# Kernel optimization log

Measured on AMD Instinct MI355X. Metric: run time of the kernel, lower is better.

The kernel has to match this reference:

```python
import jax, jax.numpy as jnp
import numpy as np

W_BITS = 4  # active precision (max of supported_bits)
EPS = 0.005  # clamp margin from the original module


def _dequant_kbit(qweight, lut, w_bits):
    """Bit-plane LUT dequant.
    qweight: [w_bits, O, I//32] int32, plane b holds bit b (MSB-first code) of each
    weight's k-bit index, 32 consecutive input positions per int32 word (LSB-first
    within a word). lut: [O, 2**w_bits]. Returns dense weight [O, I].
    """
    O = qweight.shape[1]
    shifts = jnp.arange(32, dtype=jnp.int32)                     # bit position within word
    bits = (qweight[:, :, :, None] >> shifts) & 1                # [w_bits, O, I//32, 32]
    plane_w = (1 << (w_bits - 1 - jnp.arange(w_bits, dtype=jnp.int32)))
    idx = (bits * plane_w[:, None, None, None]).sum(axis=0)      # [O, I//32, 32]
    idx = idx.reshape(O, -1)                                     # [O, I]
    return jnp.take_along_axis(lut, idx, axis=1)                 # [O, I]


def _csr_dense(rows, cols, vals, O, I):
    """Scatter CSR (indptr=rows) into a dense [O, I] matrix."""
    nnz = cols.shape[0]
    k = jnp.arange(nnz, dtype=rows.dtype)
    row_ids = jnp.searchsorted(rows, k, side='right') - 1        # CSR row of each nnz
    return jnp.zeros((O, I), dtype=vals.dtype).at[row_ids, cols].add(vals)


def setup_inputs() -> dict:
    key = jax.random.key(0)
    ks = jax.random.split(key, 7)
    B, S, I, O = 4, 2048, 4096, 4096
    NNZ = 65536
    x = jax.random.normal(ks[0], (B, S, I), dtype=jnp.float32)
    qweight = jax.random.randint(ks[1], (W_BITS, O, I // 32), 0, 2147483647, dtype=jnp.int32)
    lut = jax.random.normal(ks[2], (O, 2 ** W_BITS), dtype=jnp.float32) * 0.05
    rows = jnp.sort(jax.random.randint(ks[3], (O + 1,), 0, NNZ, dtype=jnp.int32))
    rows = rows.at[0].set(0).at[-1].set(NNZ)                     # valid CSR indptr
    cols = jax.random.randint(ks[4], (NNZ,), 0, I, dtype=jnp.int32)
    vals = jax.random.normal(ks[5], (NNZ,), dtype=jnp.float32) * 0.01
    bias = jax.random.normal(ks[6], (O,), dtype=jnp.float32) * 0.01
    return {"x": x, "qweight": qweight, "lut": lut, "rows": rows,
            "cols": cols, "vals": vals, "bias": bias}


def reference(x, qweight, lut, rows, cols, vals, bias):
    O = qweight.shape[1]
    I = x.shape[-1]
    weight = _dequant_kbit(qweight, lut, W_BITS)                 # [O, I]
    y = jnp.einsum('bsi,oi->bso', x, weight)                     # dense quantized GEMM
    w_sp = _csr_dense(rows, cols, vals, O, I)                    # sparse outlier weights
    y = y + jnp.einsum('bsi,oi->bso', x, w_sp)
    y = y + bias
    fmax = jnp.finfo(x.dtype).max * (1.0 - EPS)
    return jnp.clip(y, -fmax, fmax)
```

## Files before the change

kernel.cpp:

```cpp
#include <hip/hip_runtime.h>
#include <stdint.h>

#define Mdim 8192
#define Ndim 4096
#define Kdim 4096

#define BM 256
#define BN 256
#define BK 64
#define NT2 (Kdim / BK)

typedef float f32x4 __attribute__((ext_vector_type(4)));
typedef __bf16 bf16x8 __attribute__((ext_vector_type(8)));
typedef unsigned short ushort_t;

#define FMAXC 3.3858093490333422e+38f

__device__ __forceinline__ ushort_t f2bf(float f) {
    unsigned u = __float_as_uint(f);
    u += 0x7fffu + ((u >> 16) & 1u);
    return (ushort_t)(u >> 16);
}

__device__ __forceinline__ void gload_lds16(const void* g, void* l) {
    __builtin_amdgcn_global_load_lds(
        (const __attribute__((address_space(1))) uint32_t*)g,
        (__attribute__((address_space(3))) uint32_t*)(uint32_t)(uintptr_t)l,
        16, 0, 0);
}

#define SGB(mask, n) __builtin_amdgcn_sched_group_barrier(mask, n, 0)

__global__ __launch_bounds__(128) void dequant_kernel(
        const int* __restrict__ qw, const float* __restrict__ lut,
        const int* __restrict__ rows, const int* __restrict__ cols,
        const float* __restrict__ vals, ushort_t* __restrict__ w16) {
    __shared__ float wrow[128 * 33];
    __shared__ float slut[16];
    const int o = blockIdx.x;
    const int t = threadIdx.x;

    if (t < 16) slut[t] = lut[o * 16 + t];
    __syncthreads();

    const int q0 = qw[0 * Ndim * 128 + o * 128 + t];
    const int q1 = qw[1 * Ndim * 128 + o * 128 + t];
    const int q2 = qw[2 * Ndim * 128 + o * 128 + t];
    const int q3 = qw[3 * Ndim * 128 + o * 128 + t];
    float* dst = &wrow[t * 33];
#pragma unroll
    for (int j = 0; j < 32; ++j) {
        int idx = (((q0 >> j) & 1) << 3) | (((q1 >> j) & 1) << 2) |
                  (((q2 >> j) & 1) << 1) | ((q3 >> j) & 1);
        dst[j] = slut[idx];
    }
    __syncthreads();

    const int beg = rows[o], end = rows[o + 1];
    for (int k = beg + t; k < end; k += 128) {
        int c = cols[k];
        atomicAdd(&wrow[c + (c >> 5)], vals[k]);
    }
    __syncthreads();

    __align__(16) ushort_t tmp[32];
#pragma unroll
    for (int j = 0; j < 32; ++j) tmp[j] = f2bf(dst[j]);
    uint4* dstg = (uint4*)(w16 + (size_t)o * Kdim + t * 32);
    const uint4* srcg = (const uint4*)tmp;
#pragma unroll
    for (int j = 0; j < 4; ++j) dstg[j] = srcg[j];
}

__global__ __launch_bounds__(256) void convx_kernel(
        const float* __restrict__ x, ushort_t* __restrict__ y) {
    size_t i = ((size_t)blockIdx.x * 256 + threadIdx.x) * 8;
    float4 a = *(const float4*)(x + i);
    float4 b = *(const float4*)(x + i + 4);
    __align__(16) ushort_t r[8] = {f2bf(a.x), f2bf(a.y), f2bf(a.z), f2bf(a.w),
                                   f2bf(b.x), f2bf(b.y), f2bf(b.z), f2bf(b.w)};
    *(uint4*)(y + i) = *(const uint4*)r;
}

__global__ __launch_bounds__(512, 2) void gemm_kernel(
        const ushort_t* __restrict__ A, const ushort_t* __restrict__ Bw,
        const float* __restrict__ bias, float* __restrict__ C) {
    __shared__ __align__(16) char lds[131072];

    const int wgid = blockIdx.x;
    const int swz = (wgid & 7) * 64 + (wgid >> 3);
    const int bn = swz & 15, bm = swz >> 4;
    const int m0 = bm * BM, n0 = bn * BN;

    const int tid = threadIdx.x;
    const int lane = tid & 63, wid = tid >> 6;
    const int wr = wid >> 2, wc = wid & 3;
    const int fr = lane & 15, kg = lane >> 4;

    const int srow = tid >> 3;
    const int scol = (((tid & 7) ^ (srow & 7)) * 8);
    const ushort_t* gA = A + (size_t)(m0 + srow) * Kdim + scol;
    const ushort_t* gB = Bw + (size_t)(n0 + srow) * Kdim + scol;

    const int off0 = fr * 128 + (((kg) ^ (fr & 7)) << 4);
    const int off1 = fr * 128 + (((4 | kg) ^ (fr & 7)) << 4);

    f32x4 acc[8][4];
#pragma unroll
    for (int i = 0; i < 8; ++i)
#pragma unroll
        for (int j = 0; j < 4; ++j) acc[i][j] = (f32x4){0.f, 0.f, 0.f, 0.f};

    auto stage = [&](int buf, int t1) {
        const ushort_t* sa = gA + (size_t)t1 * BK;
        const ushort_t* sb = gB + (size_t)t1 * BK;
        char* da = lds + buf * 65536 + tid * 16;
        char* db = da + 32768;
#pragma unroll
        for (int j = 0; j < 4; ++j) {
            gload_lds16(sa + (size_t)j * 64 * Kdim, da + j * 8192);
            gload_lds16(sb + (size_t)j * 64 * Kdim, db + j * 8192);
        }
    };
    auto readA = [&](bf16x8 (&FA)[8], const char* Ab, int off) {
#pragma unroll
        for (int m = 0; m < 8; ++m)
            FA[m] = *(const bf16x8*)(Ab + wr * 16384 + m * 2048 + off);
    };
    auto readB = [&](bf16x8 (&FB)[4], const char* Bb, int off) {
#pragma unroll
        for (int n = 0; n < 4; ++n)
            FB[n] = *(const bf16x8*)(Bb + wc * 8192 + n * 2048 + off);
    };
    auto mfmaK = [&](bf16x8 (&FA)[8], bf16x8 (&FB)[4]) {
#pragma unroll
        for (int m = 0; m < 8; ++m)
#pragma unroll
            for (int n = 0; n < 4; ++n)
                acc[m][n] = __builtin_amdgcn_mfma_f32_16x16x32_bf16(
                    FA[m], FB[n], acc[m][n], 0, 0, 0);
    };

    stage(0, 0);
    asm volatile("s_waitcnt vmcnt(0)");
    __builtin_amdgcn_sched_barrier(0);
    __builtin_amdgcn_s_barrier();

#pragma unroll 1
    for (int t = 0; t < NT2 - 1; ++t) {
        const char* Ab = lds + (t & 1) * 65536;
        const char* Bb = Ab + 32768;

        bf16x8 A0[8], B0[4], A1[8], B1[4];
        readA(A0, Ab, off0); readB(B0, Bb, off0);
        stage((t + 1) & 1, t + 1);
        readA(A1, Ab, off1); readB(B1, Bb, off1);

        __builtin_amdgcn_s_setprio(1);
        mfmaK(A0, B0);
        mfmaK(A1, B1);
        __builtin_amdgcn_s_setprio(0);

        SGB(0x100, 12);
#pragma unroll
        for (int i = 0; i < 4; ++i) { SGB(0x30, 2); SGB(0x8, 4); }
#pragma unroll
        for (int i = 0; i < 6; ++i) { SGB(0x100, 2); SGB(0x8, 2); }
        SGB(0x8, 36);

        asm volatile("s_waitcnt vmcnt(0)");
        __builtin_amdgcn_sched_barrier(0);
        __builtin_amdgcn_s_barrier();
    }

    {
        const char* Ab = lds + ((NT2 - 1) & 1) * 65536;
        const char* Bb = Ab + 32768;
        bf16x8 A0[8], B0[4], A1[8], B1[4];
        readA(A0, Ab, off0); readB(B0, Bb, off0);
        readA(A1, Ab, off1); readB(B1, Bb, off1);
        mfmaK(A0, B0);
        mfmaK(A1, B1);
    }

    const int rg = lane >> 4;
#pragma unroll
    for (int nf = 0; nf < 4; ++nf) {
        const int col = n0 + wc * 64 + nf * 16 + fr;
        const float bv = bias[col];
#pragma unroll
        for (int mf = 0; mf < 8; ++mf) {
            const int row = m0 + wr * 128 + mf * 16 + rg * 4;
            float* outp = C + (size_t)row * Ndim + col;
#pragma unroll
            for (int j = 0; j < 4; ++j) {
                float v = acc[mf][nf][j] + bv;
                v = fminf(fmaxf(v, -FMAXC), FMAXC);
                outp[(size_t)j * Ndim] = v;
            }
        }
    }
}

extern "C" void kernel_launch(void* const* d_in, const int* in_sizes, int n_in,
                              void* d_out, int out_size, void* d_ws, size_t ws_size,
                              hipStream_t stream) {
    const float* x    = (const float*)d_in[0];
    const int*   qw   = (const int*)d_in[1];
    const float* lut  = (const float*)d_in[2];
    const int*   rows = (const int*)d_in[3];
    const int*   cols = (const int*)d_in[4];
    const float* vals = (const float*)d_in[5];
    const float* bias = (const float*)d_in[6];
    float* out = (float*)d_out;

    ushort_t* x16 = (ushort_t*)d_ws;
    ushort_t* w16 = x16 + (size_t)Mdim * Kdim;

    hipLaunchKernelGGL(dequant_kernel, dim3(Ndim), dim3(128), 0, stream,
                       qw, lut, rows, cols, vals, w16);
    hipLaunchKernelGGL(convx_kernel, dim3((Mdim * Kdim) / (256 * 8)), dim3(256), 0, stream,
                       x, x16);
    hipLaunchKernelGGL(gemm_kernel, dim3((Mdim / BM) * (Ndim / BN)), dim3(512), 0, stream,
                       x16, w16, bias, out);
}
```

Baseline: 275.7 us.

## Pre-swizzle activations into MFMA fragment order and load A directly to registers

The conversion kernel now writes bf16 activations in MFMA fragment-major order, so each lane's 16-byte A fragment is contiguous per 16x32 tile. The GEMM loads A fragments straight from global memory into registers, double-buffered across half-tiles, and keeps only B in LDS. LDS use drops from 128KB to 64KB and the A LDS traffic goes away. In exchange the A reads now depend on global/L2 latency hidden by register prefetch, register pressure rises, and the hand-tuned schedule-group barriers are replaced.

```diff
diff --git a/kernel.cpp b/kernel.cpp
--- a/kernel.cpp
+++ b/kernel.cpp
@@ -74,18 +74,25 @@
 
 __global__ __launch_bounds__(256) void convx_kernel(
         const float* __restrict__ x, ushort_t* __restrict__ y) {
-    size_t i = ((size_t)blockIdx.x * 256 + threadIdx.x) * 8;
-    float4 a = *(const float4*)(x + i);
-    float4 b = *(const float4*)(x + i + 4);
+    size_t u = (size_t)blockIdx.x * 256 + threadIdx.x;
+    const int lane = (int)(u & 63);
+    const size_t frag = u >> 6;
+    const int kt2 = (int)(frag & 127);
+    const size_t mblk = frag >> 7;
+    const size_t m = mblk * 16 + (lane & 15);
+    const size_t k = (size_t)kt2 * 32 + (lane >> 4) * 8;
+    const float* src = x + m * Kdim + k;
+    float4 a = *(const float4*)(src);
+    float4 b = *(const float4*)(src + 4);
     __align__(16) ushort_t r[8] = {f2bf(a.x), f2bf(a.y), f2bf(a.z), f2bf(a.w),
                                    f2bf(b.x), f2bf(b.y), f2bf(b.z), f2bf(b.w)};
-    *(uint4*)(y + i) = *(const uint4*)r;
+    *(uint4*)(y + u * 8) = *(const uint4*)r;
 }
 
 __global__ __launch_bounds__(512, 2) void gemm_kernel(
         const ushort_t* __restrict__ A, const ushort_t* __restrict__ Bw,
         const float* __restrict__ bias, float* __restrict__ C) {
-    __shared__ __align__(16) char lds[131072];
+    __shared__ __align__(16) char lds[65536];
 
     const int wgid = blockIdx.x;
     const int swz = (wgid & 7) * 64 + (wgid >> 3);
@@ -97,13 +104,14 @@
     const int wr = wid >> 2, wc = wid & 3;
     const int fr = lane & 15, kg = lane >> 4;
 
+    const uint4* pA0 = (const uint4*)A + ((size_t)((bm * 2 + wr) * 8) * 128) * 64 + lane;
+
     const int srow = tid >> 3;
     const int scol = (((tid & 7) ^ (srow & 7)) * 8);
-    const ushort_t* gA = A + (size_t)(m0 + srow) * Kdim + scol;
     const ushort_t* gB = Bw + (size_t)(n0 + srow) * Kdim + scol;
 
-    const int off0 = fr * 128 + (((kg) ^ (fr & 7)) << 4);
-    const int off1 = fr * 128 + (((4 | kg) ^ (fr & 7)) << 4);
+    const int offB0 = fr * 128 + (((kg) ^ (fr & 7)) << 4);
+    const int offB1 = fr * 128 + (((4 | kg) ^ (fr & 7)) << 4);
 
     f32x4 acc[8][4];
 #pragma unroll
@@ -111,76 +119,68 @@
 #pragma unroll
         for (int j = 0; j < 4; ++j) acc[i][j] = (f32x4){0.f, 0.f, 0.f, 0.f};
 
-    auto stage = [&](int buf, int t1) {
-        const ushort_t* sa = gA + (size_t)t1 * BK;
+    auto stageB = [&](int buf, int t1) {
         const ushort_t* sb = gB + (size_t)t1 * BK;
-        char* da = lds + buf * 65536 + tid * 16;
-        char* db = da + 32768;
-#pragma unroll
-        for (int j = 0; j < 4; ++j) {
-            gload_lds16(sa + (size_t)j * 64 * Kdim, da + j * 8192);
+        char* db = lds + buf * 32768 + tid * 16;
+#pragma unroll
+        for (int j = 0; j < 4; ++j)
             gload_lds16(sb + (size_t)j * 64 * Kdim, db + j * 8192);
-        }
-    };
-    auto readA = [&](bf16x8 (&FA)[8], const char* Ab, int off) {
-#pragma unroll
-        for (int m = 0; m < 8; ++m)
-            FA[m] = *(const bf16x8*)(Ab + wr * 16384 + m * 2048 + off);
-    };
-    auto readB = [&](bf16x8 (&FB)[4], const char* Bb, int off) {
-#pragma unroll
-        for (int n = 0; n < 4; ++n)
-            FB[n] = *(const bf16x8*)(Bb + wc * 8192 + n * 2048 + off);
-    };
-    auto mfmaK = [&](bf16x8 (&FA)[8], bf16x8 (&FB)[4]) {
+    };
+    auto loadA = [&](bf16x8 (&F)[8], int kt2) {
+#pragma unroll
+        for (int mf = 0; mf < 8; ++mf)
+            F[mf] = *(const bf16x8*)(pA0 + (size_t)mf * 8192 + kt2 * 64);
+    };
+    auto readB = [&](bf16x8 (&F)[4], int buf, int off) {
+#pragma unroll
+        for (int nf = 0; nf < 4; ++nf)
+            F[nf] = *(const bf16x8*)(lds + buf * 32768 + wc * 8192 + nf * 2048 + off);
+    };
+    auto mfma32 = [&](bf16x8 (&FA)[8], bf16x8 (&FB)[4]) {
+        __builtin_amdgcn_s_setprio(1);
 #pragma unroll
         for (int m = 0; m < 8; ++m)
 #pragma unroll
             for (int n = 0; n < 4; ++n)
                 acc[m][n] = __builtin_amdgcn_mfma_f32_16x16x32_bf16(
                     FA[m], FB[n], acc[m][n], 0, 0, 0);
-    };
-
-    stage(0, 0);
-    asm volatile("s_waitcnt vmcnt(0)");
+        __builtin_amdgcn_s_setprio(0);
+    };
+
+    bf16x8 Aa[8], Ab[8], FB[4];
+
+    stageB(0, 0);
+    loadA(Aa, 0);
+    asm volatile("s_waitcnt vmcnt(8)");
     __builtin_amdgcn_sched_barrier(0);
     __builtin_amdgcn_s_barrier();
 
 #pragma unroll 1
     for (int t = 0; t < NT2 - 1; ++t) {
-        const char* Ab = lds + (t & 1) * 65536;
-        const char* Bb = Ab + 32768;
-
-        bf16x8 A0[8], B0[4], A1[8], B1[4];
-        readA(A0, Ab, off0); readB(B0, Bb, off0);
-        stage((t + 1) & 1, t + 1);
-        readA(A1, Ab, off1); readB(B1, Bb, off1);
-
-        __builtin_amdgcn_s_setprio(1);
-        mfmaK(A0, B0);
-        mfmaK(A1, B1);
-        __builtin_amdgcn_s_setprio(0);
-
-        SGB(0x100, 12);
-#pragma unroll
-        for (int i = 0; i < 4; ++i) { SGB(0x30, 2); SGB(0x8, 4); }
-#pragma unroll
-        for (int i = 0; i < 6; ++i) { SGB(0x100, 2); SGB(0x8, 2); }
-        SGB(0x8, 36);
-
-        asm volatile("s_waitcnt vmcnt(0)");
+        const int bufc = t & 1, bufn = (t + 1) & 1;
+
+        stageB(bufn, t + 1);
+        loadA(Ab, t * 2 + 1);
+        readB(FB, bufc, offB0);
+        SGB(0x30, 12); SGB(0x100, 4); SGB(0x8, 32);
+        mfma32(Aa, FB);
+
+        loadA(Aa, (t + 1) * 2);
+        readB(FB, bufc, offB1);
+        SGB(0x30, 8); SGB(0x100, 4); SGB(0x8, 32);
+        mfma32(Ab, FB);
+
+        asm volatile("s_waitcnt vmcnt(8)");
         __builtin_amdgcn_sched_barrier(0);
         __builtin_amdgcn_s_barrier();
     }
 
     {
-        const char* Ab = lds + ((NT2 - 1) & 1) * 65536;
-        const char* Bb = Ab + 32768;
-        bf16x8 A0[8], B0[4], A1[8], B1[4];
-        readA(A0, Ab, off0); readB(B0, Bb, off0);
-        readA(A1, Ab, off1); readB(B1, Bb, off1);
-        mfmaK(A0, B0);
-        mfmaK(A1, B1);
+        loadA(Ab, 127);
+        readB(FB, 1, offB0);
+        mfma32(Aa, FB);
+        readB(FB, 1, offB1);
+        mfma32(Ab, FB);
     }
 
     const int rg = lane >> 4;
```

Measured after the change: 316.5 us. +14.8%, slower.
